# Performance work log

Hardware: AMD Instinct MI355X
Metric: run time of the kernel (lower is better)

The kernel has to match this reference:

```python
import jax, jax.numpy as jnp
import numpy as np

DIM = 512
MOVE_EMBED_DIM = 64
NUM_BUCKETS = 64
EMBED = 768
B = 8192
STEPS = 10


def setup_inputs() -> dict:
    key = jax.random.key(0)
    ks = jax.random.split(key, 16)
    def g(i, shape, scale=0.02):
        return jax.random.normal(ks[i], shape, jnp.float32) * scale
    return {
        "boards": jax.random.normal(ks[0], (STEPS, B, EMBED), jnp.float32),
        "flags": jax.random.randint(ks[1], (STEPS - 2, B), 0, 2).astype(bool),
        "themes": jax.random.randint(ks[2], (B,), 0, 10),
        "moves": jax.random.randint(ks[3], (B,), 0, NUM_BUCKETS),
        "start": jax.random.uniform(ks[4], (DIM,), jnp.float32),
        "red_w": g(5, (DIM, EMBED)), "red_b": jnp.zeros((DIM,), jnp.float32),
        "ca_w": g(6, (DIM, DIM)), "ca_b": jnp.zeros((DIM,), jnp.float32),
        "cb_w": g(7, (DIM, DIM)), "cb_b": jnp.zeros((DIM,), jnp.float32),
        "move_emb": g(8, (NUM_BUCKETS, MOVE_EMBED_DIM), 1.0),
        "fc1_w": g(9, (DIM, DIM + MOVE_EMBED_DIM)), "fc1_b": jnp.zeros((DIM,), jnp.float32),
        "fc2_w": g(10, (DIM, DIM)), "fc2_b": jnp.zeros((DIM,), jnp.float32),
        "fc3_w": g(11, (1024, DIM)), "fc3_b": jnp.zeros((1024,), jnp.float32),
        "fc4_w": g(12, (1024, 1024)), "fc4_b": jnp.zeros((1024,), jnp.float32),
        "fc5_w": g(13, (512, 1024)), "fc5_b": jnp.zeros((512,), jnp.float32),
        "out_w": g(14, (1, 512)), "out_b": jnp.zeros((1,), jnp.float32),
    }


def reference(boards, flags, themes, moves, start, red_w, red_b, ca_w, ca_b,
              cb_w, cb_b, move_emb, fc1_w, fc1_b, fc2_w, fc2_b, fc3_w, fc3_b,
              fc4_w, fc4_b, fc5_w, fc5_b, out_w, out_b):
    bsz = boards.shape[1]
    # boards[0:2] are never masked; boards[2:10] are zeroed where flags are False
    full_flags = jnp.concatenate([jnp.ones((2, bsz), bool), flags], axis=0)  # [10,B]
    emb = jnp.where(full_flags[:, :, None], boards, 0.0)                     # [10,B,E]
    # shared dim reducer + relu applied to all 10 positions at once
    e = jax.nn.relu(jnp.einsum('sbe,de->sbd', emb, red_w) + red_b)           # [10,B,DIM]
    # precompute combiner_b contribution for every step (batched GEMM)
    eb = jnp.einsum('sbd,kd->sbk', e, cb_w) + cb_b                           # [10,B,DIM]
    # combiner_a(start)+combiner_b(e0) == combiner_a(h0)+... with h0 = start broadcast
    h0 = jnp.broadcast_to(start, (bsz, DIM))
    def step(h, eb_t):
        return jnp.tanh(h @ ca_w.T + ca_b + eb_t), None
    h, _ = jax.lax.scan(step, h0, eb)                                        # [B,DIM]
    # dropout layers are identity in eval mode
    m = move_emb[moves]                                                      # [B,MOVE_EMBED_DIM]
    x = jax.nn.relu(jnp.concatenate([h, m], axis=-1) @ fc1_w.T + fc1_b)
    x = jax.nn.relu(x @ fc2_w.T + fc2_b)
    x = jax.nn.relu(x @ fc3_w.T + fc3_b)
    x = jax.nn.relu(x @ fc4_w.T + fc4_b)
    x = jax.nn.relu(x @ fc5_w.T + fc5_b)
    return x @ out_w.T + out_b                                               # [B,1]
```

## Files before the change

### kernel.cpp

```cpp
#include <hip/hip_runtime.h>
#include <math.h>

#define BATCH  8192
#define EMBED  768
#define DIMD   512
#define MEDIM  64
#define NSTEP  10

typedef __bf16 bf16x8 __attribute__((ext_vector_type(8)));
typedef float  f32x4  __attribute__((ext_vector_type(4)));

__device__ __forceinline__ void load16_lds(const void* g, void* l)
{
    auto* gp = (__attribute__((address_space(1))) char*)(uintptr_t)g;
    auto* lp = (__attribute__((address_space(3))) char*)(unsigned int)(uintptr_t)l;
    __builtin_amdgcn_global_load_lds(gp, lp, 16, 0, 0);
}

#define WAITV(n) asm volatile("s_waitcnt vmcnt(" #n ")" ::: "memory")

#define BN 128
#define BK 32

template<int ACT, bool ADDEB, bool GATHER, int BMT>
__global__ __launch_bounds__(256)
void gemm_bf16(const __bf16* __restrict__ A, const __bf16* __restrict__ Bt,
               const float* __restrict__ bias, const __bf16* __restrict__ add,
               const __bf16* __restrict__ me, const int* __restrict__ moves,
               __bf16* __restrict__ C, int M, int N, int K)
{
    constexpr int NG = (BMT + BN) / 16;
    constexpr int AG = BMT / 16;
    constexpr int MR = BMT / 32;
    constexpr int NC = NG / 4;

    __shared__ __bf16 lds[3][(BMT + BN) * BK];

    const int nwg  = gridDim.x * gridDim.y;
    const int orig = blockIdx.y * gridDim.x + blockIdx.x;
    const int cpx  = nwg >> 3;
    const int swz  = (orig & 7) * cpx + (orig >> 3);
    const int bx   = swz % gridDim.x;
    const int by   = swz / gridDim.x;

    const int tid  = threadIdx.x;
    const int wave = tid >> 6;
    const int lane = tid & 63;
    const int row0 = by * BMT;
    const int col0 = bx * BN;

    const int wr = (wave >> 1) * (BMT / 2);
    const int wc = (wave & 1) * 64;
    const int fr = lane & 15;
    const int q  = lane >> 4;

    const int srow = lane >> 2;
    const int skk  = (((lane & 3) ^ ((lane >> 3) & 3)) * 8);

    int mv[2] = {0, 0};
    if (GATHER) {
#pragma unroll
        for (int ci = 0; ci < 2; ++ci)
            mv[ci] = moves[row0 + (ci * 4 + wave) * 16 + srow];
    }

    auto stage_one = [&](int buf, int k0, int ci) {
        const int c = ci * 4 + wave;
        const int r = c * 16 + srow;
        const __bf16* g;
        if (c < AG) {
            if (GATHER) {
                g = (k0 < DIMD)
                    ? (A  + (size_t)(row0 + r) * DIMD + k0 + skk)
                    : (me + (size_t)mv[ci] * MEDIM + (k0 - DIMD) + skk);
            } else {
                g = A + (size_t)(row0 + r) * K + k0 + skk;
            }
        } else {
            g = Bt + (size_t)(col0 + (r - BMT)) * K + k0 + skk;
        }
        load16_lds(g, &lds[buf][c * 512]);
    };
    auto stage = [&](int buf, int k0) {
#pragma unroll
        for (int ci = 0; ci < NC; ++ci) stage_one(buf, k0, ci);
    };

    auto frag = [&](const __bf16* base, int r) -> bf16x8 {
        return *(const bf16x8*)&base[r * 32 + ((q ^ ((r >> 1) & 3)) << 3)];
    };

    f32x4 acc[MR][4] = {};

    const int NT = K / BK;
    stage(0, 0);
    stage(1, BK);

    int rd = 0;
    for (int t = 0; t < NT; ++t) {
        if (t + 1 < NT) {
            if constexpr (NC == 4) WAITV(4); else WAITV(3);
        } else {
            WAITV(0);
        }
        __builtin_amdgcn_s_barrier();
        __builtin_amdgcn_sched_barrier(0);

        const bool dost = (t + 2 < NT);
        int wrb = rd + 2; if (wrb >= 3) wrb -= 3;
        const int k0s = (t + 2) * BK;

        const __bf16* As = lds[rd];
        const __bf16* Bs = lds[rd] + BMT * BK;
        bf16x8 bfr[4];
#pragma unroll
        for (int n = 0; n < 4; ++n)
            bfr[n] = frag(Bs, wc + n * 16 + fr);

        __builtin_amdgcn_s_setprio(1);
#pragma unroll
        for (int m = 0; m < MR; ++m) {
            if (dost) {
#pragma unroll
                for (int ci = m * NC / MR; ci < (m + 1) * NC / MR; ++ci)
                    stage_one(wrb, k0s, ci);
            }
            const bf16x8 af = frag(As, wr + m * 16 + fr);
#pragma unroll
            for (int n = 0; n < 4; ++n)
                acc[m][n] = __builtin_amdgcn_mfma_f32_16x16x32_bf16(
                                af, bfr[n], acc[m][n], 0, 0, 0);
        }
        __builtin_amdgcn_s_setprio(0);

        __builtin_amdgcn_s_barrier();
        __builtin_amdgcn_sched_barrier(0);
        ++rd; if (rd >= 3) rd -= 3;
    }

#pragma unroll
    for (int m = 0; m < MR; ++m) {
#pragma unroll
        for (int n = 0; n < 4; ++n) {
            const int cc = col0 + wc + n * 16 + fr;
            const float bb = bias[cc];
#pragma unroll
            for (int j = 0; j < 4; ++j) {
                const int rr = row0 + wr + m * 16 + (lane >> 4) * 4 + j;
                float v = acc[m][n][j] + bb;
                if (ADDEB) v += (float)add[(size_t)rr * N + cc];
                if (ACT == 1) v = fmaxf(v, 0.0f);
                if (ACT == 2) {
                    const float p = __expf(2.0f * v);
                    v = 1.0f - 2.0f / (p + 1.0f);
                }
                C[(size_t)rr * N + cc] = (__bf16)v;
            }
        }
    }
}

enum : int { W_RED = 0, W_CA = 393216, W_CB = 655360, W_FC1 = 917504,
             W_FC2 = 1212416, W_FC3 = 1474560, W_FC4 = 1998848,
             W_FC5 = 3047424, W_ME = 3571712, W_TOTAL = 3575808 };

#define NB_BOARDS 30720
#define NB_W      1746
__global__ __launch_bounds__(256)
void prep(const float* __restrict__ boards, const int* __restrict__ flags,
          __bf16* __restrict__ b_all,
          const float* __restrict__ w0, const float* __restrict__ w1,
          const float* __restrict__ w2, const float* __restrict__ w3,
          const float* __restrict__ w4, const float* __restrict__ w5,
          const float* __restrict__ w6, const float* __restrict__ w7,
          const float* __restrict__ w8, __bf16* __restrict__ wpool,
          const float* __restrict__ cab, const float* __restrict__ start,
          float* __restrict__ tmp)
{
    const int bid = blockIdx.x;
    if (bid < NB_BOARDS) {
        const int idx  = bid * 256 + threadIdx.x;
        const int grow = idx / 96;
        const int s    = grow >> 13;
        const int b    = grow & 8191;
        float m = 1.0f;
        if (s >= 2) m = flags[(size_t)(s - 2) * BATCH + b] ? 1.0f : 0.0f;
        const float4 v0 = ((const float4*)boards)[(size_t)idx * 2];
        const float4 v1 = ((const float4*)boards)[(size_t)idx * 2 + 1];
        bf16x8 o;
        o[0] = (__bf16)(v0.x * m); o[1] = (__bf16)(v0.y * m);
        o[2] = (__bf16)(v0.z * m); o[3] = (__bf16)(v0.w * m);
        o[4] = (__bf16)(v1.x * m); o[5] = (__bf16)(v1.y * m);
        o[6] = (__bf16)(v1.z * m); o[7] = (__bf16)(v1.w * m);
        *(bf16x8*)(b_all + (size_t)idx * 8) = o;
    } else if (bid < NB_BOARDS + NB_W) {
        const int idx = (bid - NB_BOARDS) * 256 + threadIdx.x;
        if (idx >= W_TOTAL / 8) return;
        const int e = idx * 8;
        const float* src; int off;
        if      (e < W_CA)  { src = w0; off = W_RED; }
        else if (e < W_CB)  { src = w1; off = W_CA; }
        else if (e < W_FC1) { src = w2; off = W_CB; }
        else if (e < W_FC2) { src = w3; off = W_FC1; }
        else if (e < W_FC3) { src = w4; off = W_FC2; }
        else if (e < W_FC4) { src = w5; off = W_FC3; }
        else if (e < W_FC5) { src = w6; off = W_FC4; }
        else if (e < W_ME)  { src = w7; off = W_FC5; }
        else                { src = w8; off = W_ME; }
        const float4 v0 = ((const float4*)(src + (e - off)))[0];
        const float4 v1 = ((const float4*)(src + (e - off)))[1];
        bf16x8 o;
        o[0] = (__bf16)v0.x; o[1] = (__bf16)v0.y; o[2] = (__bf16)v0.z; o[3] = (__bf16)v0.w;
        o[4] = (__bf16)v1.x; o[5] = (__bf16)v1.y; o[6] = (__bf16)v1.z; o[7] = (__bf16)v1.w;
        *(bf16x8*)(wpool + (size_t)e) = o;
    } else {
        __shared__ float s[DIMD];
        for (int i = threadIdx.x; i < DIMD; i += 256) s[i] = start[i];
        __syncthreads();
        const int n = (bid - NB_BOARDS - NB_W) * 256 + threadIdx.x;
        const float4* w = (const float4*)(w1 + (size_t)n * DIMD);
        float acc = 0.0f;
#pragma unroll 8
        for (int k = 0; k < DIMD / 4; ++k) {
            const float4 wv = w[k];
            acc += wv.x * s[k * 4] + wv.y * s[k * 4 + 1] +
                   wv.z * s[k * 4 + 2] + wv.w * s[k * 4 + 3];
        }
        tmp[n] = acc + cab[n];
    }
}

__global__ __launch_bounds__(256)
void h1_init(const float* __restrict__ tmp, const __bf16* __restrict__ eb0,
             __bf16* __restrict__ h)
{
    const int idx = blockIdx.x * 256 + threadIdx.x;
    const int c8 = idx & 63;
    const bf16x8 e = ((const bf16x8*)eb0)[idx];
    bf16x8 o;
#pragma unroll
    for (int j = 0; j < 8; ++j) {
        const float v = tmp[c8 * 8 + j] + (float)e[j];
        const float p = __expf(2.0f * v);
        o[j] = (__bf16)(1.0f - 2.0f / (p + 1.0f));
    }
    ((bf16x8*)h)[idx] = o;
}

__global__ __launch_bounds__(256)
void out_head(const __bf16* __restrict__ x, const float* __restrict__ out_w,
              const float* __restrict__ out_b, float* __restrict__ out)
{
    const int wid  = threadIdx.x >> 6;
    const int lane = threadIdx.x & 63;
    const int row  = blockIdx.x * 4 + wid;
    const bf16x8 xv = *(const bf16x8*)(x + (size_t)row * DIMD + lane * 8);
    const float4 w0 = ((const float4*)out_w)[lane * 2];
    const float4 w1 = ((const float4*)out_w)[lane * 2 + 1];
    float s = (float)xv[0] * w0.x + (float)xv[1] * w0.y + (float)xv[2] * w0.z +
              (float)xv[3] * w0.w + (float)xv[4] * w1.x + (float)xv[5] * w1.y +
              (float)xv[6] * w1.z + (float)xv[7] * w1.w;
#pragma unroll
    for (int off = 32; off; off >>= 1) s += __shfl_down(s, off, 64);
    if (lane == 0) out[row] = s + out_b[0];
}

extern "C" void kernel_launch(void* const* d_in, const int* in_sizes, int n_in,
                              void* d_out, int out_size, void* d_ws, size_t ws_size,
                              hipStream_t stream)
{
    const float* boards  = (const float*)d_in[0];
    const int*   flags   = (const int*)  d_in[1];
    const int*   moves   = (const int*)  d_in[3];
    const float* start   = (const float*)d_in[4];
    const float* red_w   = (const float*)d_in[5];
    const float* red_b   = (const float*)d_in[6];
    const float* ca_w    = (const float*)d_in[7];
    const float* ca_b    = (const float*)d_in[8];
    const float* cb_w    = (const float*)d_in[9];
    const float* cb_b    = (const float*)d_in[10];
    const float* move_emb= (const float*)d_in[11];
    const float* fc1_w   = (const float*)d_in[12];
    const float* fc1_b   = (const float*)d_in[13];
    const float* fc2_w   = (const float*)d_in[14];
    const float* fc2_b   = (const float*)d_in[15];
    const float* fc3_w   = (const float*)d_in[16];
    const float* fc3_b   = (const float*)d_in[17];
    const float* fc4_w   = (const float*)d_in[18];
    const float* fc4_b   = (const float*)d_in[19];
    const float* fc5_w   = (const float*)d_in[20];
    const float* fc5_b   = (const float*)d_in[21];
    const float* out_w   = (const float*)d_in[22];
    const float* out_b   = (const float*)d_in[23];

    __bf16* wsb = (__bf16*)d_ws;
    __bf16* wpool  = wsb;
    __bf16* b_all  = wsb + 3575808;
    __bf16* e_all  = wsb + 66490368;
    __bf16* eb_all = wsb + 108433408;
    __bf16* hA     = wsb + 150376448;
    __bf16* hB     = wsb + 154570752;
    float*  tmpv   = (float*)(wsb + 158765056);
    __bf16* x1     = wsb + 159789056;
    __bf16* x2     = wsb + 163983360;
    __bf16* x3     = wsb + 168177664;
    __bf16* x4     = wsb + 176566272;
    __bf16* x5     = wsb + 184954880;

    const dim3 blk(256);

    prep<<<NB_BOARDS + NB_W + 2, blk, 0, stream>>>(
        boards, flags, b_all,
        red_w, ca_w, cb_w, fc1_w, fc2_w, fc3_w, fc4_w, fc5_w, move_emb, wpool,
        ca_b, start, tmpv);

    gemm_bf16<1, false, false, 128><<<dim3(4, 640), blk, 0, stream>>>(
        b_all, wpool + W_RED, red_b, nullptr, nullptr, nullptr, e_all,
        NSTEP * BATCH, DIMD, EMBED);
    gemm_bf16<0, false, false, 128><<<dim3(4, 640), blk, 0, stream>>>(
        e_all, wpool + W_CB, cb_b, nullptr, nullptr, nullptr, eb_all,
        NSTEP * BATCH, DIMD, DIMD);

    h1_init<<<2048, blk, 0, stream>>>(tmpv, eb_all, hA);

    __bf16* hcur = hA;
    __bf16* hnxt = hB;
    for (int s = 1; s < NSTEP; ++s) {
        const __bf16* ebs = eb_all + (size_t)s * BATCH * DIMD;
        gemm_bf16<2, true, false, 64><<<dim3(4, 128), blk, 0, stream>>>(
            hcur, wpool + W_CA, ca_b, ebs, nullptr, nullptr, hnxt,
            BATCH, DIMD, DIMD);
        __bf16* t = hcur; hcur = hnxt; hnxt = t;
    }

    gemm_bf16<1, false, true, 128><<<dim3(4, 64), blk, 0, stream>>>(
        hcur, wpool + W_FC1, fc1_b, nullptr, wpool + W_ME, moves, x1,
        BATCH, DIMD, DIMD + MEDIM);
    gemm_bf16<1, false, false, 128><<<dim3(4, 64), blk, 0, stream>>>(
        x1, wpool + W_FC2, fc2_b, nullptr, nullptr, nullptr, x2, BATCH, DIMD, DIMD);
    gemm_bf16<1, false, false, 128><<<dim3(8, 64), blk, 0, stream>>>(
        x2, wpool + W_FC3, fc3_b, nullptr, nullptr, nullptr, x3, BATCH, 1024, DIMD);
    gemm_bf16<1, false, false, 128><<<dim3(8, 64), blk, 0, stream>>>(
        x3, wpool + W_FC4, fc4_b, nullptr, nullptr, nullptr, x4, BATCH, 1024, 1024);
    gemm_bf16<1, false, false, 128><<<dim3(4, 64), blk, 0, stream>>>(
        x4, wpool + W_FC5, fc5_b, nullptr, nullptr, nullptr, x5, BATCH, DIMD, 1024);

    out_head<<<BATCH / 4, blk, 0, stream>>>(x5, out_w, out_b, (float*)d_out);
}
```

Baseline: 436.8 us.

## Use 256x128 tiled GEMM for big reducer/combiner GEMMs and fuse h1 init

```diff
diff --git a/kernel.cpp b/kernel.cpp
--- a/kernel.cpp
+++ b/kernel.cpp
@@ -155,6 +155,120 @@
                     v = 1.0f - 2.0f / (p + 1.0f);
                 }
                 C[(size_t)rr * N + cc] = (__bf16)v;
+            }
+        }
+    }
+}
+
+template<int ACT, bool H1>
+__global__ __launch_bounds__(512)
+void gemm256(const __bf16* __restrict__ A, const __bf16* __restrict__ Bt,
+             const float* __restrict__ bias, const float* __restrict__ tmp,
+             __bf16* __restrict__ h1out, __bf16* __restrict__ C,
+             int M, int N, int K)
+{
+    __shared__ __bf16 lds[3][(256 + 128) * 32];
+
+    const int nwg  = gridDim.x * gridDim.y;
+    const int orig = blockIdx.y * gridDim.x + blockIdx.x;
+    const int cpx  = nwg >> 3;
+    const int swz  = (orig & 7) * cpx + (orig >> 3);
+    const int bx   = swz % gridDim.x;
+    const int by   = swz / gridDim.x;
+
+    const int tid  = threadIdx.x;
+    const int wave = tid >> 6;
+    const int lane = tid & 63;
+    const int row0 = by * 256;
+    const int col0 = bx * 128;
+
+    const int wr = (wave >> 1) * 64;
+    const int wc = (wave & 1) * 64;
+    const int fr = lane & 15;
+    const int q  = lane >> 4;
+
+    const int srow = lane >> 2;
+    const int skk  = (((lane & 3) ^ ((lane >> 3) & 3)) * 8);
+
+    auto stage_one = [&](int buf, int k0, int ci) {
+        const int c = ci * 8 + wave;
+        const int r = c * 16 + srow;
+        const __bf16* g = (c < 16)
+            ? (A  + (size_t)(row0 + r) * K + k0 + skk)
+            : (Bt + (size_t)(col0 + (r - 256)) * K + k0 + skk);
+        load16_lds(g, &lds[buf][c * 512]);
+    };
+    auto stage = [&](int buf, int k0) {
+#pragma unroll
+        for (int ci = 0; ci < 3; ++ci) stage_one(buf, k0, ci);
+    };
+
+    auto frag = [&](const __bf16* base, int r) -> bf16x8 {
+        return *(const bf16x8*)&base[r * 32 + ((q ^ ((r >> 1) & 3)) << 3)];
+    };
+
+    f32x4 acc[4][4] = {};
+
+    const int NT = K / BK;
+    stage(0, 0);
+    stage(1, BK);
+
+    int rd = 0;
+    for (int t = 0; t < NT; ++t) {
+        if (t + 1 < NT) WAITV(3); else WAITV(0);
+        __builtin_amdgcn_s_barrier();
+        __builtin_amdgcn_sched_barrier(0);
+
+        const bool dost = (t + 2 < NT);
+        int wrb = rd + 2; if (wrb >= 3) wrb -= 3;
+        const int k0s = (t + 2) * BK;
+
+        const __bf16* As = lds[rd];
+        const __bf16* Bs = lds[rd] + 256 * 32;
+        bf16x8 bfr[4];
+#pragma unroll
+        for (int n = 0; n < 4; ++n)
+            bfr[n] = frag(Bs, wc + n * 16 + fr);
+
+        __builtin_amdgcn_s_setprio(1);
+#pragma unroll
+        for (int m = 0; m < 4; ++m) {
+            if (dost) {
+#pragma unroll
+                for (int ci = m * 3 / 4; ci < (m + 1) * 3 / 4; ++ci)
+                    stage_one(wrb, k0s, ci);
+            }
+            const bf16x8 af = frag(As, wr + m * 16 + fr);
+#pragma unroll
+            for (int n = 0; n < 4; ++n)
+                acc[m][n] = __builtin_amdgcn_mfma_f32_16x16x32_bf16(
+                                af, bfr[n], acc[m][n], 0, 0, 0);
+        }
+        __builtin_amdgcn_s_setprio(0);
+
+        __builtin_amdgcn_s_barrier();
+        __builtin_amdgcn_sched_barrier(0);
+        ++rd; if (rd >= 3) rd -= 3;
+    }
+
+#pragma unroll
+    for (int m = 0; m < 4; ++m) {
+#pragma unroll
+        for (int n = 0; n < 4; ++n) {
+            const int cc = col0 + wc + n * 16 + fr;
+            const float bb = bias[cc];
+#pragma unroll
+            for (int j = 0; j < 4; ++j) {
+                const int rr = row0 + wr + m * 16 + (lane >> 4) * 4 + j;
+                float v = acc[m][n][j] + bb;
+                if (ACT == 1) v = fmaxf(v, 0.0f);
+                if (H1 && rr < BATCH) {
+                    const float vv = v + tmp[cc];
+                    const float p = __expf(2.0f * vv);
+                    h1out[(size_t)rr * N + cc] = (__bf16)(1.0f - 2.0f / (p + 1.0f));
+                } else {
+                    C[(size_t)rr * N + cc] = (__bf16)v;
+                }
             }
         }
     }
@@ -231,23 +345,6 @@
 }
 
 __global__ __launch_bounds__(256)
-void h1_init(const float* __restrict__ tmp, const __bf16* __restrict__ eb0,
-             __bf16* __restrict__ h)
-{
-    const int idx = blockIdx.x * 256 + threadIdx.x;
-    const int c8 = idx & 63;
-    const bf16x8 e = ((const bf16x8*)eb0)[idx];
-    bf16x8 o;
-#pragma unroll
-    for (int j = 0; j < 8; ++j) {
-        const float v = tmp[c8 * 8 + j] + (float)e[j];
-        const float p = __expf(2.0f * v);
-        o[j] = (__bf16)(1.0f - 2.0f / (p + 1.0f));
-    }
-    ((bf16x8*)h)[idx] = o;
-}
-
-__global__ __launch_bounds__(256)
 void out_head(const __bf16* __restrict__ x, const float* __restrict__ out_w,
               const float* __restrict__ out_b, float* __restrict__ out)
 {
@@ -314,14 +411,12 @@
         red_w, ca_w, cb_w, fc1_w, fc2_w, fc3_w, fc4_w, fc5_w, move_emb, wpool,
         ca_b, start, tmpv);
 
-    gemm_bf16<1, false, false, 128><<<dim3(4, 640), blk, 0, stream>>>(
-        b_all, wpool + W_RED, red_b, nullptr, nullptr, nullptr, e_all,
+    gemm256<1, false><<<dim3(4, 320), dim3(512), 0, stream>>>(
+        b_all, wpool + W_RED, red_b, nullptr, nullptr, e_all,
         NSTEP * BATCH, DIMD, EMBED);
-    gemm_bf16<0, false, false, 128><<<dim3(4, 640), blk, 0, stream>>>(
-        e_all, wpool + W_CB, cb_b, nullptr, nullptr, nullptr, eb_all,
+    gemm256<0, true><<<dim3(4, 320), dim3(512), 0, stream>>>(
+        e_all, wpool + W_CB, cb_b, tmpv, hA, eb_all,
         NSTEP * BATCH, DIMD, DIMD);
-
-    h1_init<<<2048, blk, 0, stream>>>(tmpv, eb_all, hA);
 
     __bf16* hcur = hA;
     __bf16* hnxt = hB;
```

Result: no change. 437.7 us (+0.2%).
